# Optimization experiments

Hardware: AMD Instinct MI355X
Metric: run time of the kernel (lower is better)

## Reference

```python
import jax, jax.numpy as jnp
import numpy as np

ENTITY_TYPES = ['PER', 'ORG', 'LOC', 'MISC', 'GPE', 'DATE', 'TIME', 'MONEY', 'PERCENT',
                'FAC', 'EVENT', 'LAW', 'LANGUAGE', 'NORP', 'ORDINAL', 'CARDINAL', 'PRODUCT', 'QUANTITY']
TAGS = ['<PAD>', 'O'] + [f'{p}-{t}' for t in ENTITY_TYPES for p in ('B', 'I')]
TAG2IDX = {t: i for i, t in enumerate(TAGS)}
PAD_IDX = TAG2IDX['<PAD>']
O_IDX = TAG2IDX['O']
LAMBDA_MISS = 1.2
LAMBDA_FP = 1.0
LAMBDA_TRANSITION = 0.8
EPS = 1e-8


def _split_tag(tag):
    if tag in {'O', '<PAD>'} or '-' not in tag:
        return (tag, None)
    prefix, label = tag.split('-', 1)
    return (prefix, label)


def build_valid_transition_mask():
    n = len(TAGS)
    valid = np.zeros((n, n), dtype=np.float32)
    for prev_idx, prev_tag in enumerate(TAGS):
        prev_prefix, prev_label = _split_tag(prev_tag)
        for curr_idx, curr_tag in enumerate(TAGS):
            curr_prefix, curr_label = _split_tag(curr_tag)
            if curr_tag == '<PAD>' or curr_tag == 'O' or curr_prefix == 'B':
                ok = True
            elif curr_prefix == 'I':
                ok = (prev_prefix in {'B', 'I'}) and (prev_label == curr_label)
            else:
                ok = False
            valid[prev_idx, curr_idx] = 1.0 if ok else 0.0
    return valid


def setup_inputs() -> dict:
    key = jax.random.key(0)
    k1, k2 = jax.random.split(key)
    B, T, C = 128, 4096, len(TAGS)  # C = 38
    logits = jax.random.normal(k1, (B, T, C), dtype=jnp.float32)
    labels = jax.random.randint(k2, (B, T), 0, C, dtype=jnp.int32)
    valid_transition_mask = jnp.asarray(build_valid_transition_mask())  # [C, C]
    return {'logits': logits, 'labels': labels, 'valid_transition_mask': valid_transition_mask}


def _masked_mean(x, mask):
    # mean of x over positions where mask is True (0 if mask empty)
    cnt = jnp.sum(mask)
    return jnp.sum(jnp.where(mask, x, 0.0)) / jnp.maximum(cnt, 1).astype(x.dtype)


def reference(logits, labels, valid_transition_mask):
    # logits: [B, T, C]; labels: [B, T] int; valid_transition_mask: [C, C]
    logp = jax.nn.log_softmax(logits, axis=-1)            # [B, T, C]
    probs = jnp.exp(logp)                                  # softmax(logits)

    valid = labels != PAD_IDX                              # [B, T]
    # cross entropy with ignore_index=PAD (unweighted mean over valid tokens)
    gold_logp = jnp.take_along_axis(logp, labels[..., None], axis=-1)[..., 0]
    ce_loss = _masked_mean(-gold_logp, valid)

    p_o = probs[..., O_IDX]                                # [B, T]
    gold_entity = valid & (labels != O_IDX)
    gold_o = valid & (labels == O_IDX)

    # miss penalty: -log(1 - p_o) on gold entity tokens
    miss_penalty = _masked_mean(-jnp.log(jnp.clip(1.0 - p_o, EPS)), gold_entity)
    # false-positive penalty: -log(1 - (1 - p_o)) = -log(p_o) on gold O tokens
    fp_penalty = _masked_mean(-jnp.log(jnp.clip(p_o, EPS)), gold_o)

    # transition penalty: sum of prev_probs (outer) curr_probs over invalid (prev,curr)
    # pairs. Algebraically: prev . (invalid @ curr) per position, avoids [B,T,C,C].
    invalid = 1.0 - valid_transition_mask                  # [C, C]
    invalid_mass = jnp.einsum('btc,cd,btd->bt', probs[:, :-1, :], invalid, probs[:, 1:, :])
    tmask = valid[:, 1:] & valid[:, :-1]
    transition_penalty = _masked_mean(invalid_mass, tmask)

    return (ce_loss + LAMBDA_MISS * miss_penalty + LAMBDA_FP * fp_penalty
            + LAMBDA_TRANSITION * transition_penalty)
```

## Files before the change

kernel.cpp:

```cpp
#include <hip/hip_runtime.h>


#define NCLS 38
#define BUFF 2440

__global__ __launch_bounds__(128, 4) void ner_main(const float* __restrict__ logits,
                                                   const int* __restrict__ labels,
                                                   float* __restrict__ partials,
                                                   int ntiles) {
    __shared__ float S[2][2][BUFF];

    const int tid  = threadIdx.x;
    const int lane = tid & 63;
    const int wv   = tid >> 6;
    const int gw   = blockIdx.x * 2 + wv;
    const int nt   = 4 + (gw < (ntiles - 8192));

    long long tok0[5]; int offv[5], wrow[5], lab[5];
#pragma unroll
    for (int t = 0; t < 5; ++t) {
        const int tile = gw + 2048 * t;
        const int row  = (int)(((unsigned)tile * 64528u) >> 22);
        wrow[t] = tile - row * 65;
        tok0[t] = (long long)row * 4096 + 63 * wrow[t];
        offv[t] = ((int)tok0[t] & 1) * 2;
        lab[t]  = (t < nt) ? labels[tok0[t] + lane] : 0;
    }

    auto issue = [&](int t) {
        const float4* g4 = reinterpret_cast<const float4*>(logits + tok0[t] * NCLS - offv[t]);
        float* dst = &S[wv][t & 1][0];
        const int nf4 = 608 + (offv[t] ? 1 : 0);
#pragma unroll
        for (int i = 0; i < 10; ++i) {
            const int idx = lane + i * 64;
            if (idx < nf4)
                __builtin_amdgcn_global_load_lds(
                    (const __attribute__((address_space(1))) void*)(g4 + idx),
                    (__attribute__((address_space(3))) void*)(dst + i * 256),
                    16, 0, 0);
        }
    };

    issue(0);

    float ce_s = 0.f, mi_s = 0.f, fp_s = 0.f, tr_s = 0.f, c_cefp = 0.f, c_tr = 0.f;

#pragma unroll
    for (int t = 0; t < 5; ++t) {
        if (t >= nt) break;
        const bool more = (t + 1 < nt);
        if (more) issue(t + 1);
        if (more) asm volatile("s_waitcnt vmcnt(10)" ::: "memory");
        else      asm volatile("s_waitcnt vmcnt(0)"  ::: "memory");

        const float* sl = &S[wv][t & 1][offv[t]];
        const int l = lab[t];

        float v[NCLS];
        {
            const float2* lp = reinterpret_cast<const float2*>(sl + lane * NCLS);
            float2* vv = reinterpret_cast<float2*>(v);
#pragma unroll
            for (int i = 0; i < NCLS / 2; ++i) vv[i] = lp[i];
        }
        const float gold = sl[lane * NCLS + l];

        float s = 0.f;
#pragma unroll
        for (int c = 0; c < NCLS; ++c) { const float e = __expf(v[c]); v[c] = e; s += e; }
        const float inv = 1.f / s;
        const float lg  = __logf(s);

        const bool own = (lane < 63) || (wrow[t] == 64);
        if (own && l != 0) {
            ce_s += lg - gold; c_cefp += 1.f;
            const float po = v[1] * inv;
            if (l == 1) { fp_s -= __logf(fmaxf(po,       1e-8f)); c_cefp += 1024.f; }
            else        { mi_s -= __logf(fmaxf(1.f - po, 1e-8f)); }
        }

        const int   lnext = __shfl_down(l, 1, 64);
        const float qinv  = __shfl_down(inv, 1, 64);
        float qv[18];
#pragma unroll
        for (int j = 0; j < 18; ++j) qv[j] = __shfl_down(v[3 + 2 * j], 1, 64);

        if (lane < 63 && l != 0 && lnext != 0) {
            float m = 0.f;
#pragma unroll
            for (int j = 0; j < 18; ++j)
                m += qv[j] * (s - v[2 + 2 * j] - v[3 + 2 * j]);
            tr_s += m * inv * qinv; c_tr += 1.f;
        }
    }

    float vals[6] = {ce_s, mi_s, fp_s, tr_s, c_cefp, c_tr};
#pragma unroll
    for (int k = 0; k < 6; ++k) {
        float x = vals[k];
#pragma unroll
        for (int o = 32; o >= 1; o >>= 1) x += __shfl_down(x, o, 64);
        vals[k] = x;
    }
    if (lane == 0) {
        *reinterpret_cast<float4*>(partials + gw * 8) =
            make_float4(vals[0], vals[1], vals[2], vals[3]);
        *reinterpret_cast<float2*>(partials + gw * 8 + 4) =
            make_float2(vals[4], vals[5]);
    }
}

__global__ __launch_bounds__(1024) void ner_reduce(const float* __restrict__ partials,
                                                   float* __restrict__ out, int nwaves) {
    __shared__ float acc[7];
    const int tid = threadIdx.x;
    if (tid < 7) acc[tid] = 0.f;
    __syncthreads();
    float s_ce = 0.f, s_mi = 0.f, s_fp = 0.f, s_tr = 0.f;
    float c_ce = 0.f, c_fp = 0.f, c_tr = 0.f;
    for (int i = tid; i < nwaves; i += 1024) {
        const float4 p = *reinterpret_cast<const float4*>(partials + i * 8);
        const float2 q = *reinterpret_cast<const float2*>(partials + i * 8 + 4);
        s_ce += p.x; s_mi += p.y; s_fp += p.z; s_tr += p.w;
        const float fc = floorf(q.x * (1.f / 1024.f));
        c_fp += fc; c_ce += q.x - fc * 1024.f; c_tr += q.y;
    }
    float vals[7] = {s_ce, s_mi, s_fp, s_tr, c_ce, c_fp, c_tr};
#pragma unroll
    for (int k = 0; k < 7; ++k) {
        float x = vals[k];
#pragma unroll
        for (int o = 32; o >= 1; o >>= 1) x += __shfl_down(x, o, 64);
        if ((tid & 63) == 0) atomicAdd(&acc[k], x);
    }
    __syncthreads();
    if (tid == 0) {
        const float ce_c = acc[4], fp_c = acc[5], tr_c = acc[6];
        const float mi_c = ce_c - fp_c;
        out[0] = acc[0] / fmaxf(ce_c, 1.f) + 1.2f * (acc[1] / fmaxf(mi_c, 1.f))
               + 1.0f * (acc[2] / fmaxf(fp_c, 1.f)) + 0.8f * (acc[3] / fmaxf(tr_c, 1.f));
    }
}

extern "C" void kernel_launch(void* const* d_in, const int* in_sizes, int n_in,
                              void* d_out, int out_size, void* d_ws, size_t ws_size,
                              hipStream_t stream) {
    const float* logits = (const float*)d_in[0];
    const int*   labels = (const int*)d_in[1];
    float* partials = (float*)d_ws;

    const long long N = (long long)in_sizes[1];
    const int rows   = (int)(N / 4096);
    const int ntiles = rows * 65;
    const int nwaves = 2048;
    const int nblk   = nwaves / 2;

    hipLaunchKernelGGL(ner_main, dim3(nblk), dim3(128), 0, stream,
                       logits, labels, partials, ntiles);
    hipLaunchKernelGGL(ner_reduce, dim3(1), dim3(1024), 0, stream,
                       partials, (float*)d_out, nwaves);
}
```

Measured before the change: 117.8 us.

## Stage tiles through registers instead of async LDS loads and double the wave count

Drops the direct global-to-LDS async loads and the double-buffered shared memory. Each tile is now loaded into registers, stored into a single LDS buffer, and the next tile's register load is issued before computing the current one. The grid doubles to 4096 waves, so each wave handles 2-3 tiles instead of 4-5, and launch bounds drop to 3 blocks per CU. This trades the async-copy path for register prefetch and more parallelism, at the cost of higher register pressure and extra LDS store instructions.

```diff
diff --git a/kernel.cpp b/kernel.cpp
--- a/kernel.cpp
+++ b/kernel.cpp
@@ -2,24 +2,26 @@
 
 
 #define NCLS 38
-#define BUFF 2440
+#define BUFW 2448
+#define NWAVES 4096
+#define NBLK 2048
 
-__global__ __launch_bounds__(128, 4) void ner_main(const float* __restrict__ logits,
+__global__ __launch_bounds__(128, 3) void ner_main(const float* __restrict__ logits,
                                                    const int* __restrict__ labels,
                                                    float* __restrict__ partials,
                                                    int ntiles) {
-    __shared__ float S[2][2][BUFF];
+    __shared__ float S[2][BUFW];
 
     const int tid  = threadIdx.x;
     const int lane = tid & 63;
     const int wv   = tid >> 6;
     const int gw   = blockIdx.x * 2 + wv;
-    const int nt   = 4 + (gw < (ntiles - 8192));
+    const int nt   = 2 + (gw < (ntiles - 2 * NWAVES));
 
-    long long tok0[5]; int offv[5], wrow[5], lab[5];
+    long long tok0[3]; int offv[3], wrow[3], lab[3];
 #pragma unroll
-    for (int t = 0; t < 5; ++t) {
-        const int tile = gw + 2048 * t;
+    for (int t = 0; t < 3; ++t) {
+        const int tile = gw + NWAVES * t;
         const int row  = (int)(((unsigned)tile * 64528u) >> 22);
         wrow[t] = tile - row * 65;
         tok0[t] = (long long)row * 4096 + 63 * wrow[t];
@@ -27,35 +29,39 @@
         lab[t]  = (t < nt) ? labels[tok0[t] + lane] : 0;
     }
 
-    auto issue = [&](int t) {
+    float4 r[10];
+    auto load_tile = [&](int t) {
         const float4* g4 = reinterpret_cast<const float4*>(logits + tok0[t] * NCLS - offv[t]);
-        float* dst = &S[wv][t & 1][0];
         const int nf4 = 608 + (offv[t] ? 1 : 0);
 #pragma unroll
         for (int i = 0; i < 10; ++i) {
             const int idx = lane + i * 64;
-            if (idx < nf4)
-                __builtin_amdgcn_global_load_lds(
-                    (const __attribute__((address_space(1))) void*)(g4 + idx),
-                    (__attribute__((address_space(3))) void*)(dst + i * 256),
-                    16, 0, 0);
+            if (idx < nf4) r[i] = g4[idx];
+        }
+    };
+    auto store_tile = [&](int t) {
+        float4* l4 = reinterpret_cast<float4*>(&S[wv][0]);
+        const int nf4 = 608 + (offv[t] ? 1 : 0);
+#pragma unroll
+        for (int i = 0; i < 10; ++i) {
+            const int idx = lane + i * 64;
+            if (idx < nf4) l4[idx] = r[i];
         }
     };
 
-    issue(0);
+    load_tile(0);
 
     float ce_s = 0.f, mi_s = 0.f, fp_s = 0.f, tr_s = 0.f, c_cefp = 0.f, c_tr = 0.f;
 
 #pragma unroll
-    for (int t = 0; t < 5; ++t) {
+    for (int t = 0; t < 3; ++t) {
         if (t >= nt) break;
-        const bool more = (t + 1 < nt);
-        if (more) issue(t + 1);
-        if (more) asm volatile("s_waitcnt vmcnt(10)" ::: "memory");
-        else      asm volatile("s_waitcnt vmcnt(0)"  ::: "memory");
+        store_tile(t);
+        if (t + 1 < nt) load_tile(t + 1);
 
-        const float* sl = &S[wv][t & 1][offv[t]];
-        const int l = lab[t];
+        const float* sl = &S[wv][offv[t]];
+        const int l     = lab[t];
+        const int lnext = __shfl_down(l, 1, 64);
 
         float v[NCLS];
         {
@@ -80,8 +86,7 @@
             else        { mi_s -= __logf(fmaxf(1.f - po, 1e-8f)); }
         }
 
-        const int   lnext = __shfl_down(l, 1, 64);
-        const float qinv  = __shfl_down(inv, 1, 64);
+        const float qinv = __shfl_down(inv, 1, 64);
         float qv[18];
 #pragma unroll
         for (int j = 0; j < 18; ++j) qv[j] = __shfl_down(v[3 + 2 * j], 1, 64);
@@ -153,11 +158,9 @@
     const long long N = (long long)in_sizes[1];
     const int rows   = (int)(N / 4096);
     const int ntiles = rows * 65;
-    const int nwaves = 2048;
-    const int nblk   = nwaves / 2;
 
-    hipLaunchKernelGGL(ner_main, dim3(nblk), dim3(128), 0, stream,
+    hipLaunchKernelGGL(ner_main, dim3(NBLK), dim3(128), 0, stream,
                        logits, labels, partials, ntiles);
     hipLaunchKernelGGL(ner_reduce, dim3(1), dim3(1024), 0, stream,
-                       partials, (float*)d_out, nwaves);
+                       partials, (float*)d_out, NWAVES);
 }
```

Result: slower. 148.3 us (+25.9%).
